# Optimization experiments

Measured on AMD Instinct MI355X. Metric: run time of the kernel, lower is better.

## Reference

```python
import jax, jax.numpy as jnp
import numpy as np
from functools import partial

L, B, D_IN, D_MODEL, D_OUT, D_STATE = 2048, 8, 128, 256, 32, 16
D_INNER, DT_RANK, K_CONV = 2 * D_MODEL, D_MODEL // 16, 4
LOG2PI = float(np.log(2.0 * np.pi))


def setup_inputs() -> dict:
    key = jax.random.key(0)
    ks = jax.random.split(key, 16)
    sc = 0.02
    inp = {
        "s": jax.random.normal(ks[0], (L, B, D_IN), jnp.float32),
        "a": jax.random.normal(ks[1], (L, B, D_OUT), jnp.float32),
        # embedding linear
        "W_emb": jax.random.normal(ks[2], (D_IN, D_MODEL), jnp.float32) * sc,
        "b_emb": jnp.zeros((D_MODEL,), jnp.float32),
        # mamba block params
        "norm_w": jnp.ones((D_MODEL,), jnp.float32),
        "W_in": jax.random.normal(ks[3], (D_MODEL, 2 * D_INNER), jnp.float32) * sc,
        "conv_w": jax.random.normal(ks[4], (D_INNER, 1, K_CONV), jnp.float32) * sc,
        "conv_b": jnp.zeros((D_INNER,), jnp.float32),
        "W_x": jax.random.normal(ks[5], (D_INNER, DT_RANK + 2 * D_STATE), jnp.float32) * sc,
        "W_dt": jax.random.normal(ks[6], (DT_RANK, D_INNER), jnp.float32) * sc,
        "b_dt": jnp.full((D_INNER,), -2.0, jnp.float32),  # softplus(-2) ~ small init dt
        "A_log": jnp.broadcast_to(jnp.log(jnp.arange(1, D_STATE + 1, dtype=jnp.float32)), (D_INNER, D_STATE)).copy(),
        "D": jnp.ones((D_INNER,), jnp.float32),
        "W_out": jax.random.normal(ks[7], (D_INNER, D_MODEL), jnp.float32) * sc,
        # action head + log_std
        "W_head": jax.random.normal(ks[8], (D_MODEL, D_OUT), jnp.float32) * sc,
        "b_head": jnp.zeros((D_OUT,), jnp.float32),
        "log_std": jnp.zeros((D_OUT,), jnp.float32),
    }
    return inp


def _rmsnorm(x, w, eps=1e-5):
    return x * jax.lax.rsqrt(jnp.mean(x * x, axis=-1, keepdims=True) + eps) * w


def _silu(x):
    return x * jax.nn.sigmoid(x)


def _mamba_block(x, norm_w, W_in, conv_w, conv_b, W_x, W_dt, b_dt, A_log, D, W_out):
    # x: (B, L, d_model)
    resid = x
    xn = _rmsnorm(x, norm_w)
    xz = xn @ W_in                                  # (B, L, 2*d_inner)
    xp, z = jnp.split(xz, 2, axis=-1)
    # causal depthwise conv over time
    xc = jax.lax.conv_general_dilated(
        xp.transpose(0, 2, 1), conv_w, window_strides=(1,),
        padding=[(K_CONV - 1, 0)], feature_group_count=D_INNER,
        dimension_numbers=("NCH", "OIH", "NCH"))
    xp = _silu((xc + conv_b[None, :, None]).transpose(0, 2, 1))  # (B, L, d_inner)
    # input-dependent SSM params
    x_dbl = xp @ W_x                                # (B, L, dt_rank + 2*d_state)
    dt, Bm, Cm = jnp.split(x_dbl, [DT_RANK, DT_RANK + D_STATE], axis=-1)
    dt = jax.nn.softplus(dt @ W_dt + b_dt)          # (B, L, d_inner)
    A = -jnp.exp(A_log)                             # (d_inner, d_state)

    def step(h, t):
        dt_t, B_t, C_t, x_t = t                     # (B,d_i) (B,d_s) (B,d_s) (B,d_i)
        dA = jnp.exp(dt_t[..., None] * A)           # (B, d_inner, d_state)
        dBx = (dt_t * x_t)[..., None] * B_t[:, None, :]
        h = dA * h + dBx
        y = jnp.einsum("bds,bs->bd", h, C_t)
        return h, y

    h0 = jnp.zeros((x.shape[0], D_INNER, D_STATE), x.dtype)
    tm = lambda u: jnp.moveaxis(u, 1, 0)            # time-major
    _, ys = jax.lax.scan(step, h0, (tm(dt), tm(Bm), tm(Cm), tm(xp)))
    y = jnp.moveaxis(ys, 0, 1) + xp * D             # (B, L, d_inner)
    y = y * _silu(z)
    return y @ W_out + resid


def reference(s, a, W_emb, b_emb, norm_w, W_in, conv_w, conv_b, W_x, W_dt, b_dt,
              A_log, D, W_out, W_head, b_head, log_std):
    x = s @ W_emb + b_emb                           # (L, B, d_model)
    x = x.transpose(1, 0, 2)                        # (B, L, d_model)
    x = _mamba_block(x, norm_w, W_in, conv_w, conv_b, W_x, W_dt, b_dt, A_log, D, W_out)
    x = x.transpose(1, 0, 2)                        # (L, B, d_model)
    mu = x @ W_head + b_head                        # (L, B, d_out)
    # Normal(mu, exp(log_std)).log_prob(a).sum(-1)
    z = (a - mu) * jnp.exp(-log_std)
    logp = -0.5 * z * z - log_std - 0.5 * LOG2PI
    return logp.sum(axis=-1)                        # (L, B)
```

## Files before the change

kernel.cpp:

```cpp
#include <hip/hip_runtime.h>

typedef unsigned short u16;
typedef short bf16x8 __attribute__((ext_vector_type(8)));
typedef float floatx4 __attribute__((ext_vector_type(4)));

#define LSEQ 2048
#define BB 8
#define NTOK (LSEQ*BB)
#define DMODEL 256
#define DINNER 512
#define NSEG 128
#define SEGLEN 16

__device__ __forceinline__ float siluf(float x){ return x / (1.f + __expf(-x)); }
__device__ __forceinline__ float b2f(u16 x){ return __uint_as_float(((unsigned)x) << 16); }
__device__ __forceinline__ u16 f2b(float f){
  unsigned u = __float_as_uint(f);
  unsigned r = (u + 0x7fffu + ((u >> 16) & 1u)) >> 16;
  return (u16)r;
}

__global__ __launch_bounds__(256) void prep_k(
    const float* __restrict__ Wemb, const float* __restrict__ Win,
    const float* __restrict__ Wout, const float* __restrict__ Wx,
    const float* __restrict__ Wh,
    u16* __restrict__ WTe, u16* __restrict__ WTi, u16* __restrict__ WTo,
    u16* __restrict__ WxT, u16* __restrict__ WhT)
{
  int g = blockIdx.x, tid = threadIdx.x;
  if (g < 128) {
    int idx = g*256 + tid; int n = idx >> 7, k = idx & 127;
    WTe[idx] = f2b(Wemb[(size_t)k*256 + n]);
  } else if (g < 1152) {
    int idx = (g-128)*256 + tid; int n = idx >> 8, k = idx & 255;
    WTi[idx] = f2b(Win[(size_t)k*1024 + n]);
  } else if (g < 1664) {
    int idx = (g-1152)*256 + tid; int n = idx >> 9, k = idx & 511;
    WTo[idx] = f2b(Wout[(size_t)k*256 + n]);
  } else if (g < 1760) {
    int idx = (g-1664)*256 + tid; int n = idx >> 9, k = idx & 511;
    WxT[idx] = f2b(Wx[(size_t)k*48 + n]);
  } else {
    int idx = (g-1760)*256 + tid; int j = idx >> 8, k = idx & 255;
    WhT[idx] = f2b(Wh[(size_t)k*32 + j]);
  }
}

__global__ __launch_bounds__(256) void embnorm_k(
    const float* __restrict__ s, const u16* __restrict__ WTe,
    const float* __restrict__ bemb, const float* __restrict__ nw,
    u16* __restrict__ Xb, u16* __restrict__ XNb)
{
  __shared__ u16 SH[64*264];
  __shared__ float ssq[64*4];
  __shared__ float rr[64];
  u16* As = SH;
  u16* Bs = SH + 64*40;
  const int tid = threadIdx.x;
  const int wave = tid >> 6, lane = tid & 63;
  const int quad = lane >> 4, l16 = lane & 15;
  const int m0 = blockIdx.x*64;
  const int wn = wave*64;
  const int srow = tid >> 2, sch = (tid & 3)*8;
  floatx4 acc[4][4];
  #pragma unroll
  for (int r = 0; r < 4; ++r)
    #pragma unroll
    for (int c = 0; c < 4; ++c) acc[r][c] = (floatx4){0.f,0.f,0.f,0.f};

  for (int k0 = 0; k0 < 128; k0 += 32) {
    {
      float4 v0 = *(const float4*)&s[(size_t)(m0+srow)*128 + k0 + sch];
      float4 v1 = *(const float4*)&s[(size_t)(m0+srow)*128 + k0 + sch + 4];
      __align__(16) u16 o[8];
      o[0]=f2b(v0.x); o[1]=f2b(v0.y); o[2]=f2b(v0.z); o[3]=f2b(v0.w);
      o[4]=f2b(v1.x); o[5]=f2b(v1.y); o[6]=f2b(v1.z); o[7]=f2b(v1.w);
      *(uint4*)&As[srow*40 + sch] = *(const uint4*)o;
    }
    #pragma unroll
    for (int p = 0; p < 4; ++p) {
      int row = srow + p*64;
      *(uint4*)&Bs[row*40 + sch] = *(const uint4*)&WTe[(size_t)row*128 + k0 + sch];
    }
    __syncthreads();
    bf16x8 af[4], bf[4];
    #pragma unroll
    for (int r = 0; r < 4; ++r) af[r] = *(const bf16x8*)&As[(r*16 + l16)*40 + quad*8];
    #pragma unroll
    for (int c = 0; c < 4; ++c) bf[c] = *(const bf16x8*)&Bs[(wn + c*16 + l16)*40 + quad*8];
    #pragma unroll
    for (int r = 0; r < 4; ++r)
      #pragma unroll
      for (int c = 0; c < 4; ++c)
        acc[r][c] = __builtin_amdgcn_mfma_f32_16x16x32_bf16(af[r], bf[c], acc[r][c], 0, 0, 0);
    __syncthreads();
  }
  u16* Xs = SH;
  #pragma unroll
  for (int c = 0; c < 4; ++c) {
    int n = wn + c*16 + l16;
    float bv = bemb[n];
    #pragma unroll
    for (int r = 0; r < 4; ++r)
      #pragma unroll
      for (int reg = 0; reg < 4; ++reg) {
        int ml = r*16 + quad*4 + reg;
        Xs[ml*264 + n] = f2b(acc[r][c][reg] + bv);
      }
  }
  __syncthreads();
  #pragma unroll
  for (int p = 0; p < 8; ++p) {
    int row = p*8 + (tid >> 5);
    int col = (tid & 31)*8;
    *(uint4*)&Xb[(size_t)(m0+row)*256 + col] = *(const uint4*)&Xs[row*264 + col];
  }
  const int tk = tid >> 2, q = tid & 3;
  float ss = 0.f;
  #pragma unroll
  for (int j = 0; j < 8; ++j) {
    uint4 v = *(const uint4*)&Xs[tk*264 + q*64 + j*8];
    const u16* u = (const u16*)&v;
    #pragma unroll
    for (int i = 0; i < 8; ++i) { float x = b2f(u[i]); ss += x*x; }
  }
  ssq[tk*4 + q] = ss;
  __syncthreads();
  if (q == 0)
    rr[tk] = rsqrtf((ssq[tk*4]+ssq[tk*4+1]+ssq[tk*4+2]+ssq[tk*4+3])*(1.f/DMODEL) + 1e-5f);
  __syncthreads();
  float r = rr[tk];
  #pragma unroll
  for (int j = 0; j < 8; ++j) {
    int idx = q*64 + j*8;
    uint4 v = *(const uint4*)&Xs[tk*264 + idx];
    const u16* u = (const u16*)&v;
    float4 w0 = *(const float4*)&nw[idx];
    float4 w1 = *(const float4*)&nw[idx+4];
    __align__(16) u16 o[8];
    o[0]=f2b(b2f(u[0])*r*w0.x); o[1]=f2b(b2f(u[1])*r*w0.y);
    o[2]=f2b(b2f(u[2])*r*w0.z); o[3]=f2b(b2f(u[3])*r*w0.w);
    o[4]=f2b(b2f(u[4])*r*w1.x); o[5]=f2b(b2f(u[5])*r*w1.y);
    o[6]=f2b(b2f(u[6])*r*w1.z); o[7]=f2b(b2f(u[7])*r*w1.w);
    *(uint4*)&XNb[(size_t)(m0+tk)*256 + idx] = *(const uint4*)o;
  }
}

template<int K>
__global__ __launch_bounds__(256) void gemm_mfma(
    const u16* __restrict__ Ab, const u16* __restrict__ WT,
    u16* __restrict__ Cv, int N)
{
  __shared__ u16 SH[2*128*72];
  u16* As = SH;
  u16* Bs = SH + 128*72;
  const int tid = threadIdx.x;
  const int wave = tid >> 6, lane = tid & 63;
  const int quad = lane >> 4, l16 = lane & 15;
  const int bm0 = blockIdx.x*128, bn0 = blockIdx.y*128;
  const int wm = (wave & 1)*64, wn = (wave >> 1)*64;
  const int srow = tid >> 3, sch = (tid & 7)*8;
  floatx4 acc[4][4];
  #pragma unroll
  for (int r = 0; r < 4; ++r)
    #pragma unroll
    for (int c = 0; c < 4; ++c) acc[r][c] = (floatx4){0.f,0.f,0.f,0.f};

  for (int k0 = 0; k0 < K; k0 += 64) {
    #pragma unroll
    for (int p = 0; p < 4; ++p) {
      int row = srow + p*32;
      *(uint4*)&As[row*72 + sch] = *(const uint4*)&Ab[(size_t)(bm0+row)*K + k0 + sch];
      *(uint4*)&Bs[row*72 + sch] = *(const uint4*)&WT[(size_t)(bn0+row)*K + k0 + sch];
    }
    __syncthreads();
    #pragma unroll
    for (int ks = 0; ks < 2; ++ks) {
      bf16x8 af[4], bf[4];
      #pragma unroll
      for (int r = 0; r < 4; ++r)
        af[r] = *(const bf16x8*)&As[(wm + r*16 + l16)*72 + ks*32 + quad*8];
      #pragma unroll
      for (int c = 0; c < 4; ++c)
        bf[c] = *(const bf16x8*)&Bs[(wn + c*16 + l16)*72 + ks*32 + quad*8];
      #pragma unroll
      for (int r = 0; r < 4; ++r)
        #pragma unroll
        for (int c = 0; c < 4; ++c)
          acc[r][c] = __builtin_amdgcn_mfma_f32_16x16x32_bf16(af[r], bf[c], acc[r][c], 0, 0, 0);
    }
    __syncthreads();
  }
  u16* Cs = SH;
  #pragma unroll
  for (int c = 0; c < 4; ++c) {
    int nl = wn + c*16 + l16;
    #pragma unroll
    for (int r = 0; r < 4; ++r)
      #pragma unroll
      for (int reg = 0; reg < 4; ++reg) {
        int ml = wm + r*16 + quad*4 + reg;
        Cs[ml*136 + nl] = f2b(acc[r][c][reg]);
      }
  }
  __syncthreads();
  #pragma unroll
  for (int p = 0; p < 8; ++p) {
    int row = p*16 + (tid >> 4);
    int col = (tid & 15)*8;
    uint4 v = *(const uint4*)&Cs[row*136 + col];
    *(uint4*)&Cv[(size_t)(bm0+row)*N + bn0 + col] = v;
  }
}

__global__ __launch_bounds__(256) void xdblBC_k(const u16* __restrict__ XZb,
    const float* __restrict__ cw, const float* __restrict__ cb,
    const u16* __restrict__ WxT,
    float* __restrict__ BM, float* __restrict__ CM, float* __restrict__ DTR)
{
  __shared__ u16 As[64*40];
  __shared__ u16 Ws[48*40];
  __shared__ float CWs[512*4];
  __shared__ float CBs[512];
  const int tid = threadIdx.x;
  const int wave = tid >> 6, lane = tid & 63;
  const int quad = lane >> 4, l16 = lane & 15;
  const int m0 = blockIdx.x*64;
  const int srow = tid >> 2, sch = (tid & 3)*8;
  const int n = m0 + srow;
  for (int e = tid; e < 2048; e += 256) CWs[e] = cw[e];
  for (int e = tid; e < 512;  e += 256) CBs[e] = cb[e];
  floatx4 acc[3];
  #pragma unroll
  for (int j = 0; j < 3; ++j) acc[j] = (floatx4){0.f,0.f,0.f,0.f};
  __syncthreads();
  const bf16x8 z8 = {0,0,0,0,0,0,0,0};
  for (int k0 = 0; k0 < DINNER; k0 += 32) {
    bf16x8 t3 = *(const bf16x8*)&XZb[(size_t)n*1024 + k0 + sch];
    bf16x8 t2 = z8, t1 = z8, t0v = z8;
    if (n >= 8)  t2  = *(const bf16x8*)&XZb[(size_t)(n-8)*1024  + k0 + sch];
    if (n >= 16) t1  = *(const bf16x8*)&XZb[(size_t)(n-16)*1024 + k0 + sch];
    if (n >= 24) t0v = *(const bf16x8*)&XZb[(size_t)(n-24)*1024 + k0 + sch];
    __align__(16) u16 outa[8];
    #pragma unroll
    for (int j = 0; j < 8; ++j) {
      int c = k0 + sch + j;
      float4 wv = *(const float4*)&CWs[c*4];
      float xc = CBs[c] + wv.x*b2f((u16)t0v[j]) + wv.y*b2f((u16)t1[j])
               + wv.z*b2f((u16)t2[j]) + wv.w*b2f((u16)t3[j]);
      outa[j] = f2b(siluf(xc));
    }
    *(uint4*)&As[srow*40 + sch] = *(const uint4*)outa;
    if (tid < 192) {
      int wr = tid >> 2;
      *(uint4*)&Ws[wr*40 + sch] = *(const uint4*)&WxT[(size_t)wr*512 + k0 + sch];
    }
    __syncthreads();
    bf16x8 af = *(const bf16x8*)&As[(wave*16 + l16)*40 + quad*8];
    #pragma unroll
    for (int j = 0; j < 3; ++j) {
      bf16x8 bf = *(const bf16x8*)&Ws[(j*16 + l16)*40 + quad*8];
      acc[j] = __builtin_amdgcn_mfma_f32_16x16x32_bf16(af, bf, acc[j], 0, 0, 0);
    }
    __syncthreads();
  }
  const int tok0 = m0 + wave*16;
  #pragma unroll
  for (int reg = 0; reg < 4; ++reg) {
    size_t t = (size_t)(tok0 + quad*4 + reg);
    BM[t*16 + l16]  = acc[1][reg];
    CM[t*16 + l16]  = acc[2][reg];
    DTR[t*16 + l16] = acc[0][reg];
  }
}

__global__ __launch_bounds__(256) void scanA_k(const float* __restrict__ DTR,
    const u16* __restrict__ XZb, const float* __restrict__ BM,
    const float* __restrict__ cw, const float* __restrict__ cb,
    const float* __restrict__ Wdt, const float* __restrict__ bdt,
    const float* __restrict__ Alog, u16* __restrict__ HENDb, float* __restrict__ DTS)
{
  __shared__ __align__(16) float Bs[SEGLEN*16];
  __shared__ __align__(16) float DRs[SEGLEN*16];
  const int tid = threadIdx.x;
  const int seg = blockIdx.x, b = blockIdx.y, half = blockIdx.z;
  const int c = half*256 + tid;
  const int t0 = seg*SEGLEN;
  {
    int t = tid >> 4, s = tid & 15;
    size_t nb = ((size_t)(t0+t)*BB + b)*16 + s;
    Bs[tid]  = BM[nb];
    DRs[tid] = DTR[nb];
  }
  float As[16];
  #pragma unroll
  for (int s = 0; s < 16; ++s) As[s] = -__expf(Alog[c*16+s]);
  bool uni = true;
  #pragma unroll
  for (int s = 1; s < 16; ++s)
    uni = uni && (fabsf(As[s] - As[0]*(float)(s+1)) <= 1e-4f*(float)(s+1));
  float wdt[16];
  #pragma unroll
  for (int r = 0; r < 16; ++r) wdt[r] = Wdt[r*DINNER + c];
  const float bd = bdt[c];
  const float4 cwv = *(const float4*)&cw[c*4];
  const float cbv = cb[c];
  float h[16];
  #pragma unroll
  for (int s = 0; s < 16; ++s) h[s] = 0.f;
  float dts = 0.f;
  __syncthreads();
  const size_t base = (size_t)t0*BB + b;
  const u16* xzp = XZb + base*1024 + c;
  float w0 = (t0 >= 3) ? b2f(xzp[-(size_t)3*BB*1024]) : 0.f;
  float w1 = (t0 >= 2) ? b2f(xzp[-(size_t)2*BB*1024]) : 0.f;
  float w2 = (t0 >= 1) ? b2f(xzp[-(size_t)1*BB*1024]) : 0.f;
  float xz = b2f(xzp[0]);
  for (int t = 0; t < SEGLEN; ++t) {
    float xzn = 0.f;
    if (t+1 < SEGLEN) xzn = b2f(xzp[(size_t)(t+1)*BB*1024]);
    float dsum = bd;
    #pragma unroll
    for (int r = 0; r < 16; ++r) dsum = fmaf(DRs[t*16+r], wdt[r], dsum);
    float dt = (dsum > 20.f) ? dsum : __logf(1.f + __expf(dsum));
    float xp = siluf(cbv + cwv.x*w0 + cwv.y*w1 + cwv.z*w2 + cwv.w*xz);
    w0 = w1; w1 = w2; w2 = xz;
    dts += dt;
    float dtx = dt * xp;
    const float4 b0 = *(const float4*)&Bs[t*16+0];
    const float4 b1 = *(const float4*)&Bs[t*16+4];
    const float4 b2 = *(const float4*)&Bs[t*16+8];
    const float4 b3 = *(const float4*)&Bs[t*16+12];
    const float bv[16] = {b0.x,b0.y,b0.z,b0.w, b1.x,b1.y,b1.z,b1.w,
                          b2.x,b2.y,b2.z,b2.w, b3.x,b3.y,b3.z,b3.w};
    float dA[16];
    if (uni) {
      float p = __expf(dt*As[0]);
      dA[0] = p;
      #pragma unroll
      for (int s = 1; s < 16; ++s) dA[s] = dA[s-1]*p;
    } else {
      #pragma unroll
      for (int s = 0; s < 16; ++s) dA[s] = __expf(dt*As[s]);
    }
    #pragma unroll
    for (int s = 0; s < 16; ++s)
      h[s] = fmaf(dA[s], h[s], dtx*bv[s]);
    xz = xzn;
  }
  u16* hp = &HENDb[(((size_t)seg*BB + b)*DINNER + c)*16];
  #pragma unroll
  for (int q = 0; q < 2; ++q) {
    ushort4 v0, v1;
    v0.x = f2b(h[q*8+0]); v0.y = f2b(h[q*8+1]); v0.z = f2b(h[q*8+2]); v0.w = f2b(h[q*8+3]);
    v1.x = f2b(h[q*8+4]); v1.y = f2b(h[q*8+5]); v1.z = f2b(h[q*8+6]); v1.w = f2b(h[q*8+7]);
    *(ushort4*)&hp[q*8]     = v0;
    *(ushort4*)&hp[q*8 + 4] = v1;
  }
  DTS[((size_t)seg*BB + b)*DINNER + c] = dts;
}

__global__ __launch_bounds__(256) void stitch_k(u16* __restrict__ HENDb,
    const float* __restrict__ DTS, const float* __restrict__ Alog)
{
  int g = blockIdx.x*256 + threadIdx.x;
  int b = g >> 13;
  int rem = g & 8191;
  int cidx = rem >> 4;
  float A = -__expf(Alog[rem]);
  float h0 = 0.f;
  for (int k = 0; k < NSEG; ++k) {
    size_t idx = (((size_t)k*BB + b) << 13) + rem;
    float hend = b2f(HENDb[idx]);
    HENDb[idx] = f2b(h0);
    float dts = DTS[((size_t)k*BB + b)*DINNER + cidx];
    h0 = fmaf(__expf(dts*A), h0, hend);
  }
}

__global__ __launch_bounds__(256) void scanC_k(const float* __restrict__ DTR,
    const u16* __restrict__ XZb, const float* __restrict__ BM, const float* __restrict__ CM,
    const float* __restrict__ cw, const float* __restrict__ cb,
    const float* __restrict__ Wdt, const float* __restrict__ bdt,
    const float* __restrict__ Alog, const float* __restrict__ Dp,
    const u16* __restrict__ H0b, u16* __restrict__ YGb)
{
  __shared__ __align__(16) float Bs[SEGLEN*16];
  __shared__ __align__(16) float Cs[SEGLEN*16];
  __shared__ __align__(16) float DRs[SEGLEN*16];
  const int tid = threadIdx.x;
  const int seg = blockIdx.x, b = blockIdx.y, half = blockIdx.z;
  const int c = half*256 + tid;
  const int t0 = seg*SEGLEN;
  {
    int t = tid >> 4, s = tid & 15;
    size_t nb = ((size_t)(t0+t)*BB + b)*16 + s;
    Bs[tid]  = BM[nb];
    Cs[tid]  = CM[nb];
    DRs[tid] = DTR[nb];
  }
  float As[16];
  #pragma unroll
  for (int s = 0; s < 16; ++s) As[s] = -__expf(Alog[c*16+s]);
  bool uni = true;
  #pragma unroll
  for (int s = 1; s < 16; ++s)
    uni = uni && (fabsf(As[s] - As[0]*(float)(s+1)) <= 1e-4f*(float)(s+1));
  float wdt[16];
  #pragma unroll
  for (int r = 0; r < 16; ++r) wdt[r] = Wdt[r*DINNER + c];
  const float bd = bdt[c];
  const float4 cwv = *(const float4*)&cw[c*4];
  const float cbv = cb[c];
  float h[16];
  const u16* hp = &H0b[(((size_t)seg*BB + b)*DINNER + c)*16];
  #pragma unroll
  for (int q = 0; q < 4; ++q) {
    ushort4 hv = *(const ushort4*)&hp[q*4];
    h[q*4+0]=b2f(hv.x); h[q*4+1]=b2f(hv.y); h[q*4+2]=b2f(hv.z); h[q*4+3]=b2f(hv.w);
  }
  const float Dv = Dp[c];
  __syncthreads();
  const size_t base = (size_t)t0*BB + b;
  const u16* xzp = XZb + base*1024 + c;
  const u16* zp  = XZb + base*1024 + DINNER + c;
  u16*       ygp = YGb + base*DINNER + c;
  float w0 = (t0 >= 3) ? b2f(xzp[-(size_t)3*BB*1024]) : 0.f;
  float w1 = (t0 >= 2) ? b2f(xzp[-(size_t)2*BB*1024]) : 0.f;
  float w2 = (t0 >= 1) ? b2f(xzp[-(size_t)1*BB*1024]) : 0.f;
  float xz = b2f(xzp[0]);
  float zg = b2f(zp[0]);
  for (int t = 0; t < SEGLEN; ++t) {
    float xzn = 0.f, zgn = 0.f;
    if (t+1 < SEGLEN) {
      xzn = b2f(xzp[(size_t)(t+1)*BB*1024]);
      zgn = b2f(zp[(size_t)(t+1)*BB*1024]);
    }
    float dsum = bd;
    #pragma unroll
    for (int r = 0; r < 16; ++r) dsum = fmaf(DRs[t*16+r], wdt[r], dsum);
    float dt = (dsum > 20.f) ? dsum : __logf(1.f + __expf(dsum));
    float xp = siluf(cbv + cwv.x*w0 + cwv.y*w1 + cwv.z*w2 + cwv.w*xz);
    w0 = w1; w1 = w2; w2 = xz;
    float dtx = dt * xp;
    const float4 b0 = *(const float4*)&Bs[t*16+0];
    const float4 b1 = *(const float4*)&Bs[t*16+4];
    const float4 b2 = *(const float4*)&Bs[t*16+8];
    const float4 b3 = *(const float4*)&Bs[t*16+12];
    const float4 c0 = *(const float4*)&Cs[t*16+0];
    const float4 c1 = *(const float4*)&Cs[t*16+4];
    const float4 c2 = *(const float4*)&Cs[t*16+8];
    const float4 c3 = *(const float4*)&Cs[t*16+12];
    const float bvv[16] = {b0.x,b0.y,b0.z,b0.w, b1.x,b1.y,b1.z,b1.w,
                           b2.x,b2.y,b2.z,b2.w, b3.x,b3.y,b3.z,b3.w};
    const float cvv[16] = {c0.x,c0.y,c0.z,c0.w, c1.x,c1.y,c1.z,c1.w,
                           c2.x,c2.y,c2.z,c2.w, c3.x,c3.y,c3.z,c3.w};
    float dA[16];
    if (uni) {
      float p = __expf(dt*As[0]);
      dA[0] = p;
      #pragma unroll
      for (int s = 1; s < 16; ++s) dA[s] = dA[s-1]*p;
    } else {
      #pragma unroll
      for (int s = 0; s < 16; ++s) dA[s] = __expf(dt*As[s]);
    }
    float y0 = 0.f, y1 = 0.f, y2 = 0.f, y3 = 0.f;
    #pragma unroll
    for (int q = 0; q < 4; ++q) {
      h[q*4+0] = fmaf(dA[q*4+0], h[q*4+0], dtx*bvv[q*4+0]);
      h[q*4+1] = fmaf(dA[q*4+1], h[q*4+1], dtx*bvv[q*4+1]);
      h[q*4+2] = fmaf(dA[q*4+2], h[q*4+2], dtx*bvv[q*4+2]);
      h[q*4+3] = fmaf(dA[q*4+3], h[q*4+3], dtx*bvv[q*4+3]);
      y0 = fmaf(h[q*4+0], cvv[q*4+0], y0);
      y1 = fmaf(h[q*4+1], cvv[q*4+1], y1);
      y2 = fmaf(h[q*4+2], cvv[q*4+2], y2);
      y3 = fmaf(h[q*4+3], cvv[q*4+3], y3);
    }
    float y = (y0+y1) + (y2+y3);
    ygp[(size_t)t*BB*DINNER] = f2b((y + xp*Dv) * siluf(zg));
    xz = xzn; zg = zgn;
  }
}

__global__ __launch_bounds__(256) void outhead_k(const u16* __restrict__ YGb,
    const u16* __restrict__ WTo, const u16* __restrict__ Xb,
    const u16* __restrict__ WhT, const float* __restrict__ bh,
    const float* __restrict__ lstd, const float* __restrict__ a,
    float* __restrict__ out)
{
  __shared__ u16 SH[(64+256)*72];
  u16* As = SH;
  u16* Bs = SH + 64*72;
  const int tid = threadIdx.x;
  const int wave = tid >> 6, lane = tid & 63;
  const int quad = lane >> 4, l16 = lane & 15;
  const int m0 = blockIdx.x*64;
  const int n0 = wave*64;
  const int srow = tid >> 3, sch = (tid & 7)*8;
  floatx4 acc[4][4];
  #pragma unroll
  for (int r = 0; r < 4; ++r)
    #pragma unroll
    for (int c = 0; c < 4; ++c) acc[r][c] = (floatx4){0.f,0.f,0.f,0.f};

  for (int k0 = 0; k0 < DINNER; k0 += 64) {
    #pragma unroll
    for (int p = 0; p < 2; ++p) {
      int row = srow + p*32;
      *(uint4*)&As[row*72 + sch] = *(const uint4*)&YGb[(size_t)(m0+row)*DINNER + k0 + sch];
    }
    #pragma unroll
    for (int p = 0; p < 8; ++p) {
      int row = srow + p*32;
      *(uint4*)&Bs[row*72 + sch] = *(const uint4*)&WTo[(size_t)row*DINNER + k0 + sch];
    }
    __syncthreads();
    #pragma unroll
    for (int ks = 0; ks < 2; ++ks) {
      bf16x8 af[4], bf[4];
      #pragma unroll
      for (int r = 0; r < 4; ++r)
        af[r] = *(const bf16x8*)&As[(r*16 + l16)*72 + ks*32 + quad*8];
      #pragma unroll
      for (int c = 0; c < 4; ++c)
        bf[c] = *(const bf16x8*)&Bs[(n0 + c*16 + l16)*72 + ks*32 + quad*8];
      #pragma unroll
      for (int r = 0; r < 4; ++r)
        #pragma unroll
        for (int c = 0; c < 4; ++c)
          acc[r][c] = __builtin_amdgcn_mfma_f32_16x16x32_bf16(af[r], bf[c], acc[r][c], 0, 0, 0);
    }
    __syncthreads();
  }
  u16* Xs = SH;
  #pragma unroll
  for (int p = 0; p < 8; ++p) {
    int row = p*8 + (tid >> 5);
    int col = (tid & 31)*8;
    *(uint4*)&Xs[row*264 + col] = *(const uint4*)&Xb[(size_t)(m0+row)*256 + col];
  }
  __syncthreads();
  #pragma unroll
  for (int c = 0; c < 4; ++c) {
    int n = n0 + c*16 + l16;
    #pragma unroll
    for (int r = 0; r < 4; ++r) {
      #pragma unroll
      for (int reg = 0; reg < 4; ++reg) {
        int ml = r*16 + quad*4 + reg;
        Xs[ml*264 + n] = f2b(acc[r][c][reg] + b2f(Xs[ml*264 + n]));
      }
    }
  }
  __syncthreads();
  floatx4 mu[2];
  mu[0] = (floatx4){0.f,0.f,0.f,0.f};
  mu[1] = (floatx4){0.f,0.f,0.f,0.f};
  #pragma unroll
  for (int k0 = 0; k0 < DMODEL; k0 += 32) {
    bf16x8 axf = *(const bf16x8*)&Xs[(wave*16 + l16)*264 + k0 + quad*8];
    #pragma unroll
    for (int nt = 0; nt < 2; ++nt) {
      bf16x8 bwf = *(const bf16x8*)(WhT + (size_t)(nt*16 + l16)*DMODEL + k0 + quad*8);
      mu[nt] = __builtin_amdgcn_mfma_f32_16x16x32_bf16(axf, bwf, mu[nt], 0, 0, 0);
    }
  }
  float ls0 = lstd[l16],      els0 = __expf(-ls0), bh0 = bh[l16];
  float ls1 = lstd[16 + l16], els1 = __expf(-ls1), bh1 = bh[16 + l16];
  #pragma unroll
  for (int reg = 0; reg < 4; ++reg) {
    int tok = m0 + wave*16 + quad*4 + reg;
    float m0v = mu[0][reg] + bh0;
    float m1v = mu[1][reg] + bh1;
    float z0 = (a[(size_t)tok*32 + l16]      - m0v) * els0;
    float z1 = (a[(size_t)tok*32 + 16 + l16] - m1v) * els1;
    float t = (-0.5f*z0*z0 - ls0) + (-0.5f*z1*z1 - ls1) - 2.f*0.91893853320467274f;
    t += __shfl_xor(t, 1);
    t += __shfl_xor(t, 2);
    t += __shfl_xor(t, 4);
    t += __shfl_xor(t, 8);
    if (l16 == 0) out[tok] = t;
  }
}

extern "C" void kernel_launch(void* const* d_in, const int* in_sizes, int n_in,
                              void* d_out, int out_size, void* d_ws, size_t ws_size,
                              hipStream_t stream)
{
  const float* s    = (const float*)d_in[0];
  const float* a    = (const float*)d_in[1];
  const float* Wemb = (const float*)d_in[2];
  const float* bemb = (const float*)d_in[3];
  const float* nw   = (const float*)d_in[4];
  const float* Win  = (const float*)d_in[5];
  const float* cw   = (const float*)d_in[6];
  const float* cb   = (const float*)d_in[7];
  const float* Wx   = (const float*)d_in[8];
  const float* Wdt  = (const float*)d_in[9];
  const float* bdt  = (const float*)d_in[10];
  const float* Alog = (const float*)d_in[11];
  const float* Dp   = (const float*)d_in[12];
  const float* Wout = (const float*)d_in[13];
  const float* Wh   = (const float*)d_in[14];
  const float* bh   = (const float*)d_in[15];
  const float* lstd = (const float*)d_in[16];

  u16*   Xb   = (u16*)d_ws;
  u16*   XZb  = Xb  + (size_t)NTOK*DMODEL;
  u16*   XNb  = XZb + (size_t)NTOK*1024;
  u16*   YGb  = XNb + (size_t)NTOK*DMODEL;
  u16*   WTe  = YGb + (size_t)NTOK*DINNER;
  u16*   WTi  = WTe + 256*128;
  u16*   WTo  = WTi + 1024*256;
  u16*   WxT  = WTo + 256*512;
  u16*   WhT  = WxT + 48*512;
  u16*   HENDb= WhT + 32*256;
  float* BM   = (float*)(HENDb + (size_t)NSEG*BB*DINNER*16);
  float* CM   = BM + (size_t)NTOK*16;
  float* DTR  = CM + (size_t)NTOK*16;
  float* DTS  = DTR + (size_t)NTOK*16;
  float* out  = (float*)d_out;

  prep_k        <<<1792,        256, 0, stream>>>(Wemb, Win, Wout, Wx, Wh,
                                                  WTe, WTi, WTo, WxT, WhT);
  embnorm_k     <<<256,         256, 0, stream>>>(s, WTe, bemb, nw, Xb, XNb);
  gemm_mfma<256><<<dim3(128,8), 256, 0, stream>>>(XNb, WTi, XZb, 1024);
  xdblBC_k      <<<256,         256, 0, stream>>>(XZb, cw, cb, WxT, BM, CM, DTR);
  scanA_k       <<<dim3(NSEG,BB,2), 256, 0, stream>>>(DTR, XZb, BM, cw, cb, Wdt, bdt,
                                                      Alog, HENDb, DTS);
  stitch_k      <<<256,         256, 0, stream>>>(HENDb, DTS, Alog);
  scanC_k       <<<dim3(NSEG,BB,2), 256, 0, stream>>>(DTR, XZb, BM, CM, cw, cb, Wdt, bdt,
                                                      Alog, Dp, HENDb, YGb);
  outhead_k     <<<256,         256, 0, stream>>>(YGb, WTo, Xb, WhT, bh, lstd, a, out);
}
```

Measured before the change: 251.4 us.

## Cache dt and conv output from scanA for reuse in scanC; drop LDS staging

scanA now stores packed bf16 dt and the post-conv activation per token and channel, so scanC skips recomputing the dt projection, softplus and causal conv. Both scans read B, C and dt-rank rows straight from global memory as broadcast float4 loads instead of staging them in shared memory, which removes the barrier. The dA power chain is rewritten as a shallower tree of products. This adds an extra 32 MB write and read of the packed buffer, and rounding dt to bf16 in scanC loses precision.

```diff
diff --git a/kernel.cpp b/kernel.cpp
--- a/kernel.cpp
+++ b/kernel.cpp
@@ -278,20 +278,13 @@
     const u16* __restrict__ XZb, const float* __restrict__ BM,
     const float* __restrict__ cw, const float* __restrict__ cb,
     const float* __restrict__ Wdt, const float* __restrict__ bdt,
-    const float* __restrict__ Alog, u16* __restrict__ HENDb, float* __restrict__ DTS)
-{
-  __shared__ __align__(16) float Bs[SEGLEN*16];
-  __shared__ __align__(16) float DRs[SEGLEN*16];
+    const float* __restrict__ Alog, u16* __restrict__ HENDb, float* __restrict__ DTS,
+    unsigned* __restrict__ DXb)
+{
   const int tid = threadIdx.x;
   const int seg = blockIdx.x, b = blockIdx.y, half = blockIdx.z;
   const int c = half*256 + tid;
   const int t0 = seg*SEGLEN;
-  {
-    int t = tid >> 4, s = tid & 15;
-    size_t nb = ((size_t)(t0+t)*BB + b)*16 + s;
-    Bs[tid]  = BM[nb];
-    DRs[tid] = DTR[nb];
-  }
   float As[16];
   #pragma unroll
   for (int s = 0; s < 16; ++s) As[s] = -__expf(Alog[c*16+s]);
@@ -309,7 +302,6 @@
   #pragma unroll
   for (int s = 0; s < 16; ++s) h[s] = 0.f;
   float dts = 0.f;
-  __syncthreads();
   const size_t base = (size_t)t0*BB + b;
   const u16* xzp = XZb + base*1024 + c;
   float w0 = (t0 >= 3) ? b2f(xzp[-(size_t)3*BB*1024]) : 0.f;
@@ -319,26 +311,40 @@
   for (int t = 0; t < SEGLEN; ++t) {
     float xzn = 0.f;
     if (t+1 < SEGLEN) xzn = b2f(xzp[(size_t)(t+1)*BB*1024]);
+    size_t nb16 = ((size_t)(t0+t)*BB + b)*16;
+    const float4 b0 = *(const float4*)&BM[nb16+0];
+    const float4 b1 = *(const float4*)&BM[nb16+4];
+    const float4 b2 = *(const float4*)&BM[nb16+8];
+    const float4 b3 = *(const float4*)&BM[nb16+12];
+    const float4 d0 = *(const float4*)&DTR[nb16+0];
+    const float4 d1 = *(const float4*)&DTR[nb16+4];
+    const float4 d2 = *(const float4*)&DTR[nb16+8];
+    const float4 d3 = *(const float4*)&DTR[nb16+12];
     float dsum = bd;
-    #pragma unroll
-    for (int r = 0; r < 16; ++r) dsum = fmaf(DRs[t*16+r], wdt[r], dsum);
+    dsum = fmaf(d0.x,wdt[0],dsum);  dsum = fmaf(d0.y,wdt[1],dsum);
+    dsum = fmaf(d0.z,wdt[2],dsum);  dsum = fmaf(d0.w,wdt[3],dsum);
+    dsum = fmaf(d1.x,wdt[4],dsum);  dsum = fmaf(d1.y,wdt[5],dsum);
+    dsum = fmaf(d1.z,wdt[6],dsum);  dsum = fmaf(d1.w,wdt[7],dsum);
+    dsum = fmaf(d2.x,wdt[8],dsum);  dsum = fmaf(d2.y,wdt[9],dsum);
+    dsum = fmaf(d2.z,wdt[10],dsum); dsum = fmaf(d2.w,wdt[11],dsum);
+    dsum = fmaf(d3.x,wdt[12],dsum); dsum = fmaf(d3.y,wdt[13],dsum);
+    dsum = fmaf(d3.z,wdt[14],dsum); dsum = fmaf(d3.w,wdt[15],dsum);
     float dt = (dsum > 20.f) ? dsum : __logf(1.f + __expf(dsum));
     float xp = siluf(cbv + cwv.x*w0 + cwv.y*w1 + cwv.z*w2 + cwv.w*xz);
     w0 = w1; w1 = w2; w2 = xz;
     dts += dt;
+    DXb[(((size_t)(t0+t)*BB + b)*DINNER + c)] = ((unsigned)f2b(xp) << 16) | f2b(dt);
     float dtx = dt * xp;
-    const float4 b0 = *(const float4*)&Bs[t*16+0];
-    const float4 b1 = *(const float4*)&Bs[t*16+4];
-    const float4 b2 = *(const float4*)&Bs[t*16+8];
-    const float4 b3 = *(const float4*)&Bs[t*16+12];
     const float bv[16] = {b0.x,b0.y,b0.z,b0.w, b1.x,b1.y,b1.z,b1.w,
                           b2.x,b2.y,b2.z,b2.w, b3.x,b3.y,b3.z,b3.w};
     float dA[16];
     if (uni) {
       float p = __expf(dt*As[0]);
-      dA[0] = p;
-      #pragma unroll
-      for (int s = 1; s < 16; ++s) dA[s] = dA[s-1]*p;
+      float p2 = p*p, p4 = p2*p2, p8 = p4*p4;
+      dA[0]=p;      dA[1]=p2;     dA[2]=p2*p;   dA[3]=p4;
+      dA[4]=p4*p;   dA[5]=p4*p2;  dA[6]=p4*p2*p;dA[7]=p8;
+      dA[8]=p8*p;   dA[9]=p8*p2;  dA[10]=p8*p2*p; dA[11]=p8*p4;
+      dA[12]=p8*p4*p; dA[13]=p8*p4*p2; dA[14]=p8*p4*p2*p; dA[15]=p8*p8;
     } else {
       #pragma unroll
       for (int s = 0; s < 16; ++s) dA[s] = __expf(dt*As[s]);
@@ -378,27 +384,15 @@
   }
 }
 
-__global__ __launch_bounds__(256) void scanC_k(const float* __restrict__ DTR,
+__global__ __launch_bounds__(256) void scanC_k(const unsigned* __restrict__ DXb,
     const u16* __restrict__ XZb, const float* __restrict__ BM, const float* __restrict__ CM,
-    const float* __restrict__ cw, const float* __restrict__ cb,
-    const float* __restrict__ Wdt, const float* __restrict__ bdt,
     const float* __restrict__ Alog, const float* __restrict__ Dp,
     const u16* __restrict__ H0b, u16* __restrict__ YGb)
 {
-  __shared__ __align__(16) float Bs[SEGLEN*16];
-  __shared__ __align__(16) float Cs[SEGLEN*16];
-  __shared__ __align__(16) float DRs[SEGLEN*16];
   const int tid = threadIdx.x;
   const int seg = blockIdx.x, b = blockIdx.y, half = blockIdx.z;
   const int c = half*256 + tid;
   const int t0 = seg*SEGLEN;
-  {
-    int t = tid >> 4, s = tid & 15;
-    size_t nb = ((size_t)(t0+t)*BB + b)*16 + s;
-    Bs[tid]  = BM[nb];
-    Cs[tid]  = CM[nb];
-    DRs[tid] = DTR[nb];
-  }
   float As[16];
   #pragma unroll
   for (int s = 0; s < 16; ++s) As[s] = -__expf(Alog[c*16+s]);
@@ -406,12 +400,6 @@
   #pragma unroll
   for (int s = 1; s < 16; ++s)
     uni = uni && (fabsf(As[s] - As[0]*(float)(s+1)) <= 1e-4f*(float)(s+1));
-  float wdt[16];
-  #pragma unroll
-  for (int r = 0; r < 16; ++r) wdt[r] = Wdt[r*DINNER + c];
-  const float bd = bdt[c];
-  const float4 cwv = *(const float4*)&cw[c*4];
-  const float cbv = cb[c];
   float h[16];
   const u16* hp = &H0b[(((size_t)seg*BB + b)*DINNER + c)*16];
   #pragma unroll
@@ -420,47 +408,42 @@
     h[q*4+0]=b2f(hv.x); h[q*4+1]=b2f(hv.y); h[q*4+2]=b2f(hv.z); h[q*4+3]=b2f(hv.w);
   }
   const float Dv = Dp[c];
-  __syncthreads();
   const size_t base = (size_t)t0*BB + b;
-  const u16* xzp = XZb + base*1024 + c;
+  const unsigned* dxp = DXb + base*DINNER + c;
   const u16* zp  = XZb + base*1024 + DINNER + c;
   u16*       ygp = YGb + base*DINNER + c;
-  float w0 = (t0 >= 3) ? b2f(xzp[-(size_t)3*BB*1024]) : 0.f;
-  float w1 = (t0 >= 2) ? b2f(xzp[-(size_t)2*BB*1024]) : 0.f;
-  float w2 = (t0 >= 1) ? b2f(xzp[-(size_t)1*BB*1024]) : 0.f;
-  float xz = b2f(xzp[0]);
+  unsigned dx = dxp[0];
   float zg = b2f(zp[0]);
   for (int t = 0; t < SEGLEN; ++t) {
-    float xzn = 0.f, zgn = 0.f;
+    unsigned dxn = 0; float zgn = 0.f;
     if (t+1 < SEGLEN) {
-      xzn = b2f(xzp[(size_t)(t+1)*BB*1024]);
+      dxn = dxp[(size_t)(t+1)*BB*DINNER];
       zgn = b2f(zp[(size_t)(t+1)*BB*1024]);
     }
-    float dsum = bd;
-    #pragma unroll
-    for (int r = 0; r < 16; ++r) dsum = fmaf(DRs[t*16+r], wdt[r], dsum);
-    float dt = (dsum > 20.f) ? dsum : __logf(1.f + __expf(dsum));
-    float xp = siluf(cbv + cwv.x*w0 + cwv.y*w1 + cwv.z*w2 + cwv.w*xz);
-    w0 = w1; w1 = w2; w2 = xz;
-    float dtx = dt * xp;
-    const float4 b0 = *(const float4*)&Bs[t*16+0];
-    const float4 b1 = *(const float4*)&Bs[t*16+4];
-    const float4 b2 = *(const float4*)&Bs[t*16+8];
-    const float4 b3 = *(const float4*)&Bs[t*16+12];
-    const float4 c0 = *(const float4*)&Cs[t*16+0];
-    const float4 c1 = *(const float4*)&Cs[t*16+4];
-    const float4 c2 = *(const float4*)&Cs[t*16+8];
-    const float4 c3 = *(const float4*)&Cs[t*16+12];
+    float dt = __uint_as_float(dx << 16);
+    float xp = __uint_as_float(dx & 0xffff0000u);
+    size_t nb16 = ((size_t)(t0+t)*BB + b)*16;
+    const float4 b0 = *(const float4*)&BM[nb16+0];
+    const float4 b1 = *(const float4*)&BM[nb16+4];
+    const float4 b2 = *(const float4*)&BM[nb16+8];
+    const float4 b3 = *(const float4*)&BM[nb16+12];
+    const float4 c0 = *(const float4*)&CM[nb16+0];
+    const float4 c1 = *(const float4*)&CM[nb16+4];
+    const float4 c2 = *(const float4*)&CM[nb16+8];
+    const float4 c3 = *(const float4*)&CM[nb16+12];
     const float bvv[16] = {b0.x,b0.y,b0.z,b0.w, b1.x,b1.y,b1.z,b1.w,
                            b2.x,b2.y,b2.z,b2.w, b3.x,b3.y,b3.z,b3.w};
     const float cvv[16] = {c0.x,c0.y,c0.z,c0.w, c1.x,c1.y,c1.z,c1.w,
                            c2.x,c2.y,c2.z,c2.w, c3.x,c3.y,c3.z,c3.w};
+    float dtx = dt * xp;
     float dA[16];
     if (uni) {
       float p = __expf(dt*As[0]);
-      dA[0] = p;
-      #pragma unroll
-      for (int s = 1; s < 16; ++s) dA[s] = dA[s-1]*p;
+      float p2 = p*p, p4 = p2*p2, p8 = p4*p4;
+      dA[0]=p;      dA[1]=p2;     dA[2]=p2*p;   dA[3]=p4;
+      dA[4]=p4*p;   dA[5]=p4*p2;  dA[6]=p4*p2*p;dA[7]=p8;
+      dA[8]=p8*p;   dA[9]=p8*p2;  dA[10]=p8*p2*p; dA[11]=p8*p4;
+      dA[12]=p8*p4*p; dA[13]=p8*p4*p2; dA[14]=p8*p4*p2*p; dA[15]=p8*p8;
     } else {
       #pragma unroll
       for (int s = 0; s < 16; ++s) dA[s] = __expf(dt*As[s]);
@@ -479,7 +462,7 @@
     }
     float y = (y0+y1) + (y2+y3);
     ygp[(size_t)t*BB*DINNER] = f2b((y + xp*Dv) * siluf(zg));
-    xz = xzn; zg = zgn;
+    dx = dxn; zg = zgn;
   }
 }
 
@@ -616,7 +599,8 @@
   u16*   WxT  = WTo + 256*512;
   u16*   WhT  = WxT + 48*512;
   u16*   HENDb= WhT + 32*256;
-  float* BM   = (float*)(HENDb + (size_t)NSEG*BB*DINNER*16);
+  unsigned* DXb = (unsigned*)(HENDb + (size_t)NSEG*BB*DINNER*16);
+  float* BM   = (float*)(DXb + (size_t)NTOK*DINNER);
   float* CM   = BM + (size_t)NTOK*16;
   float* DTR  = CM + (size_t)NTOK*16;
   float* DTS  = DTR + (size_t)NTOK*16;
@@ -628,9 +612,9 @@
   gemm_mfma<256><<<dim3(128,8), 256, 0, stream>>>(XNb, WTi, XZb, 1024);
   xdblBC_k      <<<256,         256, 0, stream>>>(XZb, cw, cb, WxT, BM, CM, DTR);
   scanA_k       <<<dim3(NSEG,BB,2), 256, 0, stream>>>(DTR, XZb, BM, cw, cb, Wdt, bdt,
-                                                      Alog, HENDb, DTS);
+                                                      Alog, HENDb, DTS, DXb);
   stitch_k      <<<256,         256, 0, stream>>>(HENDb, DTS, Alog);
-  scanC_k       <<<dim3(NSEG,BB,2), 256, 0, stream>>>(DTR, XZb, BM, CM, cw, cb, Wdt, bdt,
+  scanC_k       <<<dim3(NSEG,BB,2), 256, 0, stream>>>(DXb, XZb, BM, CM,
                                                       Alog, Dp, HENDb, YGb);
   outhead_k     <<<256,         256, 0, stream>>>(YGb, WTo, Xb, WhT, bh, lstd, a, out);
 }
```

After: 248.4 us. About the same (-1.2%).
